# Optimization experiments

Hardware: AMD Instinct MI355X
Metric: run time of the kernel (lower is better)

Reference implementation:

```python
import jax, jax.numpy as jnp
import numpy as np

EMBED_DIM = 1024

def setup_inputs() -> dict:
    key = jax.random.key(0)
    kx, kq, kk, kv = jax.random.split(key, 4)
    scale = 1.0 / np.sqrt(EMBED_DIM)  # Kaiming-uniform-ish init scale
    x = jax.random.normal(kx, (4, 2048, EMBED_DIM), dtype=jnp.float32)
    Wq = jax.random.uniform(kq, (EMBED_DIM, EMBED_DIM), jnp.float32, -scale, scale)
    Wk = jax.random.uniform(kk, (EMBED_DIM, EMBED_DIM), jnp.float32, -scale, scale)
    Wv = jax.random.uniform(kv, (EMBED_DIM, EMBED_DIM), jnp.float32, -scale, scale)
    return {"x": x, "Wq": Wq, "Wk": Wk, "Wv": Wv}

def reference(x, Wq, Wk, Wv):
    # Linear layers: y = x @ W.T (torch nn.Linear convention, no bias)
    q = jnp.einsum('bsd,ed->bse', x, Wq)
    k = jnp.einsum('bsd,ed->bse', x, Wk)
    v = jnp.einsum('bsd,ed->bse', x, Wv)
    d = k.shape[-1]
    scores = jnp.einsum('bqe,bke->bqk', q, k) / jnp.sqrt(jnp.asarray(d, x.dtype))
    attn = jax.nn.softmax(scores, axis=-1)
    return jnp.einsum('bqk,bke->bqe', attn, v)
```

## Files before the change

### kernel.cpp

```cpp
#include <hip/hip_runtime.h>
#include <hip/hip_bf16.h>

typedef unsigned short u16;
typedef __bf16 bf16x8 __attribute__((ext_vector_type(8)));
typedef float f32x4 __attribute__((ext_vector_type(4)));

__device__ __forceinline__ u16 f2bf(float f) {
    unsigned int u = __builtin_bit_cast(unsigned int, f);
    unsigned int r = u + 0x7FFFu + ((u >> 16) & 1u);
    return (u16)(r >> 16);
}

__device__ __forceinline__ float bf2f(unsigned int bits16) {
    return __builtin_bit_cast(float, bits16 << 16);
}

__device__ __forceinline__ void gload_lds16(const u16* g, u16* l) {
    __builtin_amdgcn_global_load_lds(
        (const __attribute__((address_space(1))) void*)(g),
        (__attribute__((address_space(3))) void*)(l), 16, 0, 0);
}

__global__ __launch_bounds__(256) void cvt_bf16_kernel(
    const float* __restrict__ in, u16* __restrict__ out, int n8)
{
    int i = blockIdx.x * 256 + threadIdx.x;
    if (i >= n8) return;
    const float4* p = (const float4*)in + 2 * (long long)i;
    float4 a = p[0], b = p[1];
    uint4 o;
    o.x = (unsigned)f2bf(a.x) | ((unsigned)f2bf(a.y) << 16);
    o.y = (unsigned)f2bf(a.z) | ((unsigned)f2bf(a.w) << 16);
    o.z = (unsigned)f2bf(b.x) | ((unsigned)f2bf(b.y) << 16);
    o.w = (unsigned)f2bf(b.z) | ((unsigned)f2bf(b.w) << 16);
    ((uint4*)out)[i] = o;
}

__global__ __launch_bounds__(256) void cvt3_bf16_kernel(
    const float* __restrict__ a, const float* __restrict__ b,
    const float* __restrict__ c, u16* __restrict__ out, int n8per)
{
    int i = blockIdx.x * 256 + threadIdx.x;
    if (i >= n8per) return;
    const float* in = (blockIdx.y == 0) ? a : ((blockIdx.y == 1) ? b : c);
    const float4* p = (const float4*)in + 2 * (long long)i;
    float4 va = p[0], vb = p[1];
    uint4 o;
    o.x = (unsigned)f2bf(va.x) | ((unsigned)f2bf(va.y) << 16);
    o.y = (unsigned)f2bf(va.z) | ((unsigned)f2bf(va.w) << 16);
    o.z = (unsigned)f2bf(vb.x) | ((unsigned)f2bf(vb.y) << 16);
    o.w = (unsigned)f2bf(vb.z) | ((unsigned)f2bf(vb.w) << 16);
    ((uint4*)(out + (long long)blockIdx.y * n8per * 8))[i] = o;
}

__global__ __launch_bounds__(256) void inv_rows(
    const float* __restrict__ partial, float* __restrict__ inv, int n)
{
    int i = blockIdx.x * 256 + threadIdx.x;
    if (i >= n) return;
    const float* p = partial + (long long)i * 8;
    float s = 0.f;
#pragma unroll
    for (int k = 0; k < 8; ++k) s += p[k];
    inv[i] = 1.0f / s;
}

template <int BN, bool OUT_F32, int EPI>
__global__ __launch_bounds__(512, 2) void gemm4p(
    const u16* __restrict__ A, const u16* __restrict__ B, void* __restrict__ Cv,
    int lda, int ldb, int ldc, int K,
    long long sAz, long long sBz, long long sCz, int cw, int ch,
    float* __restrict__ aux)
{
    constexpr int WC = (BN == 256) ? 4 : 2;
    constexpr int ROWS = (BN == 256) ? 128 : 64;
    constexpr int MI = ROWS / 16;
    constexpr int MIh = MI / 2;
    constexpr int BLOADS = BN / 64;
    constexpr int BNK = BN * 64;

    extern __shared__ u16 lds[];
    u16* ldsB = lds + 32768;

    const int flat = blockIdx.x + gridDim.x * blockIdx.y;
    const int xcd = flat & 7, jj = flat >> 3;
    const int nCx = gridDim.x / cw;
    const int bx = (xcd % nCx) * cw + jj % cw;
    const int by = (xcd / nCx) * ch + jj / cw;

    const int z = blockIdx.z;
    A += (long long)z * sAz;
    B += (long long)z * sBz;

    const int tid  = threadIdx.x;
    const int lane = tid & 63;
    const int wave = tid >> 6;
    const int wr = wave / WC, wc = wave % WC;
    const int m0 = by << 8, n0 = bx * BN;
    const int NT = K >> 6;

    const u16* gAp[4];
    const u16* gBp[BLOADS];
#pragma unroll
    for (int i = 0; i < 4; ++i) {
        int s = tid + i * 512, row = ((s >> 7) << 4) | (s & 15), g = (s >> 4) & 7;
        gAp[i] = A + (long long)(m0 + row) * lda + g * 8;
    }
#pragma unroll
    for (int i = 0; i < BLOADS; ++i) {
        int s = tid + i * 512, row = ((s >> 7) << 4) | (s & 15), g = (s >> 4) & 7;
        gBp[i] = B + (long long)(n0 + row) * ldb + g * 8;
    }
    auto stA = [&](int kt, int buf, int i) {
        gload_lds16(gAp[i] + (long long)kt * 64, lds + buf * 16384 + (tid + i * 512) * 8);
    };
    auto stB = [&](int kt, int buf, int i) {
        gload_lds16(gBp[i] + (long long)kt * 64, ldsB + buf * BNK + (tid + i * 512) * 8);
    };

    f32x4 acc[MI][4] = {};

#pragma unroll
    for (int i = 0; i < 4; ++i) stA(0, 0, i);
#pragma unroll
    for (int i = 0; i < BLOADS; ++i) stB(0, 0, i);
#pragma unroll
    for (int i = 0; i < 4; ++i) stA(1, 1, i);
#pragma unroll
    for (int i = 0; i < BLOADS; ++i) stB(1, 1, i);
    if constexpr (BN == 256) asm volatile("s_waitcnt vmcnt(8)" ::: "memory");
    else                     asm volatile("s_waitcnt vmcnt(6)" ::: "memory");
    __builtin_amdgcn_s_barrier();

    for (int kt = 0; kt < NT; ++kt) {
        const int cur = kt & 1;
        const u16* sAc = lds  + cur * 16384 + lane * 8;
        const u16* sBc = ldsB + cur * BNK   + lane * 8;
        const bool st = (kt + 2 < NT);

        bf16x8 a[MIh][2], b0[2][2], b1[2][2];

#pragma unroll
        for (int mi = 0; mi < MIh; ++mi)
#pragma unroll
            for (int kk = 0; kk < 2; ++kk)
                a[mi][kk] = *(const bf16x8*)(sAc + ((wr * MI + mi) * 8 + kk * 4) * 128);
#pragma unroll
        for (int ni = 0; ni < 2; ++ni)
#pragma unroll
            for (int kk = 0; kk < 2; ++kk)
                b0[ni][kk] = *(const bf16x8*)(sBc + ((wc * 4 + ni) * 8 + kk * 4) * 128);
        __builtin_amdgcn_s_barrier();
        asm volatile("s_waitcnt lgkmcnt(0)" ::: "memory");
        __builtin_amdgcn_s_setprio(1);
#pragma unroll
        for (int kk = 0; kk < 2; ++kk)
#pragma unroll
            for (int mi = 0; mi < MIh; ++mi)
#pragma unroll
                for (int ni = 0; ni < 2; ++ni)
                    acc[mi][ni] = __builtin_amdgcn_mfma_f32_16x16x32_bf16(
                        a[mi][kk], b0[ni][kk], acc[mi][ni], 0, 0, 0);
        __builtin_amdgcn_s_setprio(0);
        __builtin_amdgcn_s_barrier();

#pragma unroll
        for (int ni = 0; ni < 2; ++ni)
#pragma unroll
            for (int kk = 0; kk < 2; ++kk)
                b1[ni][kk] = *(const bf16x8*)(sBc + ((wc * 4 + 2 + ni) * 8 + kk * 4) * 128);
        if constexpr (BN == 256) {
            if (st) { stA(kt + 2, cur, 0); stA(kt + 2, cur, 2); }
        }
        __builtin_amdgcn_s_barrier();
        asm volatile("s_waitcnt lgkmcnt(0)" ::: "memory");
        __builtin_amdgcn_s_setprio(1);
#pragma unroll
        for (int kk = 0; kk < 2; ++kk)
#pragma unroll
            for (int mi = 0; mi < MIh; ++mi)
#pragma unroll
                for (int ni = 0; ni < 2; ++ni)
                    acc[mi][2 + ni] = __builtin_amdgcn_mfma_f32_16x16x32_bf16(
                        a[mi][kk], b1[ni][kk], acc[mi][2 + ni], 0, 0, 0);
        __builtin_amdgcn_s_setprio(0);
        __builtin_amdgcn_s_barrier();

#pragma unroll
        for (int mi = 0; mi < MIh; ++mi)
#pragma unroll
            for (int kk = 0; kk < 2; ++kk)
                a[mi][kk] = *(const bf16x8*)(sAc + ((wr * MI + MIh + mi) * 8 + kk * 4) * 128);
        if (st) {
            if constexpr (BN == 256) { stB(kt + 2, cur, 0); stB(kt + 2, cur, 1); }
            else                     { stB(kt + 2, cur, 0); }
        }
        __builtin_amdgcn_s_barrier();
        asm volatile("s_waitcnt lgkmcnt(0)" ::: "memory");
        __builtin_amdgcn_s_setprio(1);
#pragma unroll
        for (int kk = 0; kk < 2; ++kk)
#pragma unroll
            for (int mi = 0; mi < MIh; ++mi)
#pragma unroll
                for (int ni = 0; ni < 2; ++ni)
                    acc[MIh + mi][ni] = __builtin_amdgcn_mfma_f32_16x16x32_bf16(
                        a[mi][kk], b0[ni][kk], acc[MIh + mi][ni], 0, 0, 0);
        __builtin_amdgcn_s_setprio(0);
        __builtin_amdgcn_s_barrier();

        if (st) {
            if constexpr (BN == 256) {
                stA(kt + 2, cur, 1); stA(kt + 2, cur, 3);
                stB(kt + 2, cur, 2); stB(kt + 2, cur, 3);
            } else {
                stA(kt + 2, cur, 0); stA(kt + 2, cur, 1);
                stA(kt + 2, cur, 2); stA(kt + 2, cur, 3);
                stB(kt + 2, cur, 1);
            }
        }
        __builtin_amdgcn_s_barrier();
        __builtin_amdgcn_s_setprio(1);
#pragma unroll
        for (int kk = 0; kk < 2; ++kk)
#pragma unroll
            for (int mi = 0; mi < MIh; ++mi)
#pragma unroll
                for (int ni = 0; ni < 2; ++ni)
                    acc[MIh + mi][2 + ni] = __builtin_amdgcn_mfma_f32_16x16x32_bf16(
                        a[mi][kk], b1[ni][kk], acc[MIh + mi][2 + ni], 0, 0, 0);
        __builtin_amdgcn_s_setprio(0);
        if (st) {
            if constexpr (BN == 256) asm volatile("s_waitcnt vmcnt(8)" ::: "memory");
            else                     asm volatile("s_waitcnt vmcnt(6)" ::: "memory");
        } else if (kt + 1 < NT) {
            asm volatile("s_waitcnt vmcnt(0)" ::: "memory");
        }
        __builtin_amdgcn_s_barrier();
    }

    const int fl = lane & 15, fg = lane >> 4;
    const int er0 = m0 + wr * ROWS + fg * 4;
    const int ec0 = n0 + wc * 64 + fl;

    if constexpr (EPI == 1) {
        u16* C = (u16*)Cv + (long long)z * sCz;
        float lsum[MI][4];
#pragma unroll
        for (int mi = 0; mi < MI; ++mi)
#pragma unroll
            for (int j = 0; j < 4; ++j) {
                float s = 0.f;
#pragma unroll
                for (int ni = 0; ni < 4; ++ni) {
                    float e = __expf(acc[mi][ni][j] * 0.03125f);
                    u16 h = f2bf(e);
                    C[(long long)(er0 + mi * 16 + j) * ldc + ec0 + ni * 16] = h;
                    s += bf2f(h);
                }
                lsum[mi][j] = s;
            }
#pragma unroll
        for (int mi = 0; mi < MI; ++mi)
#pragma unroll
            for (int j = 0; j < 4; ++j)
#pragma unroll
                for (int off = 1; off < 16; off <<= 1)
                    lsum[mi][j] += __shfl_xor(lsum[mi][j], off, 64);
        float (*rsbuf)[4] = reinterpret_cast<float(*)[4]>(lds);
        if (fl == 0) {
#pragma unroll
            for (int mi = 0; mi < MI; ++mi)
#pragma unroll
                for (int j = 0; j < 4; ++j)
                    rsbuf[wr * ROWS + mi * 16 + fg * 4 + j][wc] = lsum[mi][j];
        }
        __syncthreads();
        if (tid < 256) {
            float s = rsbuf[tid][0] + rsbuf[tid][1] + rsbuf[tid][2] + rsbuf[tid][3];
            aux[((long long)z * 2048 + m0 + tid) * 8 + bx] = s;
        }
    } else if constexpr (EPI == 2) {
        float* C = (float*)Cv + (long long)z * sCz;
        float iv[MI][4];
#pragma unroll
        for (int mi = 0; mi < MI; ++mi)
#pragma unroll
            for (int j = 0; j < 4; ++j)
                iv[mi][j] = aux[(long long)z * 2048 + er0 + mi * 16 + j];
#pragma unroll
        for (int mi = 0; mi < MI; ++mi)
#pragma unroll
            for (int ni = 0; ni < 4; ++ni)
#pragma unroll
                for (int j = 0; j < 4; ++j)
                    C[(long long)(er0 + mi * 16 + j) * ldc + ec0 + ni * 16] =
                        acc[mi][ni][j] * iv[mi][j];
    } else if constexpr (OUT_F32) {
        float* C = (float*)Cv + (long long)z * sCz;
#pragma unroll
        for (int mi = 0; mi < MI; ++mi)
#pragma unroll
            for (int ni = 0; ni < 4; ++ni)
#pragma unroll
                for (int j = 0; j < 4; ++j)
                    C[(long long)(er0 + mi * 16 + j) * ldc + ec0 + ni * 16] = acc[mi][ni][j];
    } else {
        u16* C = (u16*)Cv + (long long)z * sCz;
#pragma unroll
        for (int mi = 0; mi < MI; ++mi)
#pragma unroll
            for (int ni = 0; ni < 4; ++ni)
#pragma unroll
                for (int j = 0; j < 4; ++j)
                    C[(long long)(er0 + mi * 16 + j) * ldc + ec0 + ni * 16] = f2bf(acc[mi][ni][j]);
    }
}

extern "C" void kernel_launch(void* const* d_in, const int* in_sizes, int n_in,
                              void* d_out, int out_size, void* d_ws, size_t ws_size,
                              hipStream_t stream) {
    const float* x  = (const float*)d_in[0];
    const float* Wq = (const float*)d_in[1];
    const float* Wk = (const float*)d_in[2];
    const float* Wv = (const float*)d_in[3];
    float* out = (float*)d_out;

    const int B = 4, S = 2048, D = 1024;
    const long long MS = (long long)B * S;

    u16* Sc  = (u16*)d_ws;
    u16* xb  = Sc;
    u16* wqk = Sc  + (long long)B * S * S;
    u16* wvb = wqk + 2 * D * D;
    u16* qk  = wvb + D * D;
    u16* vT  = qk  + MS * 2 * D;
    float* partial = (float*)(vT + MS * D);
    float* inv     = partial + (long long)MS * 8;
    size_t need = (size_t)2 * ((long long)B * S * S + 3 * D * D + MS * 2 * D + MS * D)
                + (size_t)4 * (MS * 8 + MS);
    if (ws_size < need) return;

    hipFuncSetAttribute(reinterpret_cast<const void*>(&gemm4p<256, false, 0>),
                        hipFuncAttributeMaxDynamicSharedMemorySize, 131072);
    hipFuncSetAttribute(reinterpret_cast<const void*>(&gemm4p<128, false, 0>),
                        hipFuncAttributeMaxDynamicSharedMemorySize, 98304);
    hipFuncSetAttribute(reinterpret_cast<const void*>(&gemm4p<256, false, 1>),
                        hipFuncAttributeMaxDynamicSharedMemorySize, 131072);
    hipFuncSetAttribute(reinterpret_cast<const void*>(&gemm4p<128, true, 2>),
                        hipFuncAttributeMaxDynamicSharedMemorySize, 98304);

    cvt_bf16_kernel<<<(int)(MS * D / 8 / 256), 256, 0, stream>>>(x, xb, (int)(MS * D / 8));
    cvt3_bf16_kernel<<<dim3(D * D / 8 / 256, 3, 1), 256, 0, stream>>>(
        Wq, Wk, Wv, wqk, D * D / 8);

    gemm4p<256, false, 0><<<dim3(2 * D / 256, (int)(MS / 256), 1), 512, 131072, stream>>>(
        xb, wqk, qk, D, D, 2 * D, D, 0, 0, 0, 8, 4, nullptr);

    gemm4p<128, false, 0><<<dim3((int)(MS / 128), D / 256, 1), 512, 98304, stream>>>(
        wvb, xb, vT, D, D, (int)MS, D, 0, 0, 0, 8, 4, nullptr);

    gemm4p<256, false, 1><<<dim3(S / 256, S / 256, B), 512, 131072, stream>>>(
        qk, qk + D, Sc, 2 * D, 2 * D, S, D,
        (long long)S * 2 * D, (long long)S * 2 * D, (long long)S * S, 2, 4, partial);

    inv_rows<<<(int)(MS / 256), 256, 0, stream>>>(partial, inv, (int)MS);

    gemm4p<128, true, 2><<<dim3(D / 128, S / 256, B), 512, 98304, stream>>>(
        Sc, vT, out, S, (int)MS, D, S,
        (long long)S * S, (long long)S, (long long)S * D, 4, 2, inv);
}
```

Before: 182.7 us.

## Merge conversion kernels, fold row-sum reduction into PV epilogue, reorder prefetch issue

```diff
diff --git a/kernel.cpp b/kernel.cpp
--- a/kernel.cpp
+++ b/kernel.cpp
@@ -21,48 +21,31 @@
         (__attribute__((address_space(3))) void*)(l), 16, 0, 0);
 }
 
-__global__ __launch_bounds__(256) void cvt_bf16_kernel(
-    const float* __restrict__ in, u16* __restrict__ out, int n8)
+__global__ __launch_bounds__(256) void cvt_all(
+    const float* __restrict__ x, const float* __restrict__ Wq,
+    const float* __restrict__ Wk, const float* __restrict__ Wv,
+    u16* __restrict__ xb, u16* __restrict__ wqkv)
 {
-    int i = blockIdx.x * 256 + threadIdx.x;
-    if (i >= n8) return;
-    const float4* p = (const float4*)in + 2 * (long long)i;
-    float4 a = p[0], b = p[1];
+    long long b = blockIdx.x;
+    const float* src;
+    u16* dst;
+    long long i8;
+    if (b < 4096) {
+        src = x; dst = xb; i8 = b * 256 + threadIdx.x;
+    } else {
+        int wsel = (int)((b - 4096) >> 9);
+        src = (wsel == 0) ? Wq : ((wsel == 1) ? Wk : Wv);
+        dst = wqkv + (long long)wsel * 1024 * 1024;
+        i8 = ((b - 4096) & 511) * 256 + threadIdx.x;
+    }
+    const float4* p = (const float4*)src + 2 * i8;
+    float4 a = p[0], c = p[1];
     uint4 o;
     o.x = (unsigned)f2bf(a.x) | ((unsigned)f2bf(a.y) << 16);
     o.y = (unsigned)f2bf(a.z) | ((unsigned)f2bf(a.w) << 16);
-    o.z = (unsigned)f2bf(b.x) | ((unsigned)f2bf(b.y) << 16);
-    o.w = (unsigned)f2bf(b.z) | ((unsigned)f2bf(b.w) << 16);
-    ((uint4*)out)[i] = o;
-}
-
-__global__ __launch_bounds__(256) void cvt3_bf16_kernel(
-    const float* __restrict__ a, const float* __restrict__ b,
-    const float* __restrict__ c, u16* __restrict__ out, int n8per)
-{
-    int i = blockIdx.x * 256 + threadIdx.x;
-    if (i >= n8per) return;
-    const float* in = (blockIdx.y == 0) ? a : ((blockIdx.y == 1) ? b : c);
-    const float4* p = (const float4*)in + 2 * (long long)i;
-    float4 va = p[0], vb = p[1];
-    uint4 o;
-    o.x = (unsigned)f2bf(va.x) | ((unsigned)f2bf(va.y) << 16);
-    o.y = (unsigned)f2bf(va.z) | ((unsigned)f2bf(va.w) << 16);
-    o.z = (unsigned)f2bf(vb.x) | ((unsigned)f2bf(vb.y) << 16);
-    o.w = (unsigned)f2bf(vb.z) | ((unsigned)f2bf(vb.w) << 16);
-    ((uint4*)(out + (long long)blockIdx.y * n8per * 8))[i] = o;
-}
-
-__global__ __launch_bounds__(256) void inv_rows(
-    const float* __restrict__ partial, float* __restrict__ inv, int n)
-{
-    int i = blockIdx.x * 256 + threadIdx.x;
-    if (i >= n) return;
-    const float* p = partial + (long long)i * 8;
-    float s = 0.f;
-#pragma unroll
-    for (int k = 0; k < 8; ++k) s += p[k];
-    inv[i] = 1.0f / s;
+    o.z = (unsigned)f2bf(c.x) | ((unsigned)f2bf(c.y) << 16);
+    o.w = (unsigned)f2bf(c.z) | ((unsigned)f2bf(c.w) << 16);
+    ((uint4*)dst)[i8] = o;
 }
 
 template <int BN, bool OUT_F32, int EPI>
@@ -132,6 +115,7 @@
     else                     asm volatile("s_waitcnt vmcnt(6)" ::: "memory");
     __builtin_amdgcn_s_barrier();
 
+#pragma unroll 2
     for (int kt = 0; kt < NT; ++kt) {
         const int cur = kt & 1;
         const u16* sAc = lds  + cur * 16384 + lane * 8;
@@ -164,14 +148,14 @@
         __builtin_amdgcn_s_setprio(0);
         __builtin_amdgcn_s_barrier();
 
+        if constexpr (BN == 256) {
+            if (st) { stA(kt + 2, cur, 0); stA(kt + 2, cur, 2); }
+        }
 #pragma unroll
         for (int ni = 0; ni < 2; ++ni)
 #pragma unroll
             for (int kk = 0; kk < 2; ++kk)
                 b1[ni][kk] = *(const bf16x8*)(sBc + ((wc * 4 + 2 + ni) * 8 + kk * 4) * 128);
-        if constexpr (BN == 256) {
-            if (st) { stA(kt + 2, cur, 0); stA(kt + 2, cur, 2); }
-        }
         __builtin_amdgcn_s_barrier();
         asm volatile("s_waitcnt lgkmcnt(0)" ::: "memory");
         __builtin_amdgcn_s_setprio(1);
@@ -186,15 +170,15 @@
         __builtin_amdgcn_s_setprio(0);
         __builtin_amdgcn_s_barrier();
 
-#pragma unroll
-        for (int mi = 0; mi < MIh; ++mi)
-#pragma unroll
-            for (int kk = 0; kk < 2; ++kk)
-                a[mi][kk] = *(const bf16x8*)(sAc + ((wr * MI + MIh + mi) * 8 + kk * 4) * 128);
         if (st) {
             if constexpr (BN == 256) { stB(kt + 2, cur, 0); stB(kt + 2, cur, 1); }
             else                     { stB(kt + 2, cur, 0); }
         }
+#pragma unroll
+        for (int mi = 0; mi < MIh; ++mi)
+#pragma unroll
+            for (int kk = 0; kk < 2; ++kk)
+                a[mi][kk] = *(const bf16x8*)(sAc + ((wr * MI + MIh + mi) * 8 + kk * 4) * 128);
         __builtin_amdgcn_s_barrier();
         asm volatile("s_waitcnt lgkmcnt(0)" ::: "memory");
         __builtin_amdgcn_s_setprio(1);
@@ -286,8 +270,13 @@
 #pragma unroll
         for (int mi = 0; mi < MI; ++mi)
 #pragma unroll
-            for (int j = 0; j < 4; ++j)
-                iv[mi][j] = aux[(long long)z * 2048 + er0 + mi * 16 + j];
+            for (int j = 0; j < 4; ++j) {
+                const float* pr = aux + ((long long)z * 2048 + er0 + mi * 16 + j) * 8;
+                float s = 0.f;
+#pragma unroll
+                for (int k = 0; k < 8; ++k) s += pr[k];
+                iv[mi][j] = 1.0f / s;
+            }
 #pragma unroll
         for (int mi = 0; mi < MI; ++mi)
 #pragma unroll
@@ -336,23 +325,20 @@
     u16* qk  = wvb + D * D;
     u16* vT  = qk  + MS * 2 * D;
     float* partial = (float*)(vT + MS * D);
-    float* inv     = partial + (long long)MS * 8;
     size_t need = (size_t)2 * ((long long)B * S * S + 3 * D * D + MS * 2 * D + MS * D)
-                + (size_t)4 * (MS * 8 + MS);
+                + (size_t)4 * (MS * 8);
     if (ws_size < need) return;
 
     hipFuncSetAttribute(reinterpret_cast<const void*>(&gemm4p<256, false, 0>),
+                        hipFuncAttributeMaxDynamicSharedMemorySize, 131072);
+    hipFuncSetAttribute(reinterpret_cast<const void*>(&gemm4p<256, false, 1>),
                         hipFuncAttributeMaxDynamicSharedMemorySize, 131072);
     hipFuncSetAttribute(reinterpret_cast<const void*>(&gemm4p<128, false, 0>),
                         hipFuncAttributeMaxDynamicSharedMemorySize, 98304);
-    hipFuncSetAttribute(reinterpret_cast<const void*>(&gemm4p<256, false, 1>),
-                        hipFuncAttributeMaxDynamicSharedMemorySize, 131072);
     hipFuncSetAttribute(reinterpret_cast<const void*>(&gemm4p<128, true, 2>),
                         hipFuncAttributeMaxDynamicSharedMemorySize, 98304);
 
-    cvt_bf16_kernel<<<(int)(MS * D / 8 / 256), 256, 0, stream>>>(x, xb, (int)(MS * D / 8));
-    cvt3_bf16_kernel<<<dim3(D * D / 8 / 256, 3, 1), 256, 0, stream>>>(
-        Wq, Wk, Wv, wqk, D * D / 8);
+    cvt_all<<<4096 + 3 * 512, 256, 0, stream>>>(x, Wq, Wk, Wv, xb, wqk);
 
     gemm4p<256, false, 0><<<dim3(2 * D / 256, (int)(MS / 256), 1), 512, 131072, stream>>>(
         xb, wqk, qk, D, D, 2 * D, D, 0, 0, 0, 8, 4, nullptr);
@@ -364,9 +350,7 @@
         qk, qk + D, Sc, 2 * D, 2 * D, S, D,
         (long long)S * 2 * D, (long long)S * 2 * D, (long long)S * S, 2, 4, partial);
 
-    inv_rows<<<(int)(MS / 256), 256, 0, stream>>>(partial, inv, (int)MS);
-
     gemm4p<128, true, 2><<<dim3(D / 128, S / 256, B), 512, 98304, stream>>>(
         Sc, vT, out, S, (int)MS, D, S,
-        (long long)S * S, (long long)S, (long long)S * D, 4, 2, inv);
-}
+        (long long)S * S, (long long)S, (long long)S * D, 4, 2, partial);
+}
```

Measured after the change: 180.2 us. About the same (-1.4%).
